# Kernel tuning notes

Hardware: AMD Instinct MI355X
Metric: run time of the kernel (lower is better)

The kernel has to match this reference:

```python
import jax, jax.numpy as jnp
import numpy as np

# Conv2d config matching init_kwargs
STRIDE = (1, 1)
PADDING = (1, 1)
DILATION = (1, 1)


def setup_inputs() -> dict:
    key = jax.random.key(0)
    k1, k2, k3 = jax.random.split(key, 3)
    B, Cin, H, W_ = 32, 128, 56, 56
    Cout, KH, KW = 256, 3, 3
    x = jax.random.normal(k1, (B, Cin, H, W_), dtype=jnp.float32)
    # original init: uniform(-stdv, stdv), stdv = 1/sqrt(Cin*KH*KW)
    stdv = 1.0 / np.sqrt(Cin * KH * KW)
    W = jax.random.uniform(k2, (Cout, Cin, KH, KW), dtype=jnp.float32, minval=-stdv, maxval=stdv)
    b = jax.random.uniform(k3, (Cout,), dtype=jnp.float32, minval=-stdv, maxval=stdv)
    return {"x": x, "W": W, "b": b}


def reference(x, W, b):
    # Same math as unfold(im2col) + GEMM + bias: a standard 2D convolution.
    out = jax.lax.conv_general_dilated(
        x, W,
        window_strides=STRIDE,
        padding=[(PADDING[0], PADDING[0]), (PADDING[1], PADDING[1])],
        rhs_dilation=DILATION,
        dimension_numbers=("NCHW", "OIHW", "NCHW"),
    )
    return out + b[None, :, None, None]
```

## Files before the change

kernel.cpp:

```cpp
#include <hip/hip_runtime.h>

typedef unsigned short ushort_t;
typedef __attribute__((ext_vector_type(8))) short bf16x8;
typedef __attribute__((ext_vector_type(4))) float f32x4;
typedef __attribute__((ext_vector_type(4))) unsigned short ushort4v;

constexpr int BATCH = 32, CIN = 128, H = 56, W = 56, COUT = 256;
constexpr int HP = 58, WP = 58;
constexpr int KTOT = CIN * 9;
constexpr size_t WB_BYTES = (size_t)COUT * KTOT * 2;
constexpr int PLANE = BATCH * HP * WP;
constexpr size_t XP_BYTES = (size_t)16 * PLANE * 8 * 2;

__device__ inline ushort_t f2bf(float f) {
  union { float fl; unsigned u; } v; v.fl = f;
  unsigned u = v.u;
  return (ushort_t)((u + 0x7fffu + ((u >> 16) & 1u)) >> 16);
}


__global__ void conv_w(const float* __restrict__ Ws, ushort_t* __restrict__ Wb2) {
  int idx = blockIdx.x * 256 + threadIdx.x;
  int c = idx & 7;
  int cout = (idx >> 3) & 255;
  int kb = (idx >> 11) & 7;
  int t = idx >> 14;
  int pos = t >> 1, half = t & 1;
  int cin = half * 64 + kb * 8 + c;
  Wb2[idx] = f2bf(Ws[(cout * 128 + cin) * 9 + pos]);
}

__global__ void xpad2(const float* __restrict__ x, ushort_t* __restrict__ xp2) {
  __shared__ ushort_t tile[128][58];
  int bh = blockIdx.x;
  int b = bh / 58, h = bh - b * 58;
  bool interior = (h >= 1 && h <= 56);
  if (interior) {
    int hIn = h - 1;
    const float4* x4 = (const float4*)x;
    {
      int ch = threadIdx.x & 127, side = threadIdx.x >> 7;
      tile[ch][side * 57] = 0;
    }
    for (int it = 0; it < 7; ++it) {
      int i = it * 256 + (int)threadIdx.x;
      int ch = i / 14, q = i - ch * 14;
      float4 v = x4[(size_t)(b * 128 + ch) * 784 + hIn * 14 + q];
      int wb = 1 + q * 4;
      tile[ch][wb + 0] = f2bf(v.x);
      tile[ch][wb + 1] = f2bf(v.y);
      tile[ch][wb + 2] = f2bf(v.z);
      tile[ch][wb + 3] = f2bf(v.w);
    }
  }
  __syncthreads();
  ushort4v* o4 = (ushort4v*)xp2;
  for (int it = 0; it < 8; ++it) {
    int i = it * 256 + (int)threadIdx.x;
    if (i >= 1856) break;
    int c8 = i / 116, r = i - c8 * 116;
    int w = r >> 1, hf = r & 1;
    ushort4v v;
    if (interior) {
      int ch = c8 * 8 + hf * 4;
      v.x = tile[ch + 0][w];
      v.y = tile[ch + 1][w];
      v.z = tile[ch + 2][w];
      v.w = tile[ch + 3][w];
    } else {
      v.x = v.y = v.z = v.w = 0;
    }
    o4[((size_t)((c8 * 32 + b) * 58 + h) * 58 + w) * 2 + hf] = v;
  }
}


__global__ __launch_bounds__(512) void conv_mfma(
    const ushort_t* __restrict__ Wb2, const ushort_t* __restrict__ xp2,
    const float* __restrict__ bias, float* __restrict__ out) {
  __shared__ ushort_t ldsA[2][16384];
  __shared__ ushort_t ldsB[2][16384];

  const int tid = threadIdx.x;
  const int lane = tid & 63;
  const int wid = tid >> 6;
  const int wm = wid >> 2, wn = wid & 3;
  const int lg = lane >> 4, lr = lane & 15;
  const int tileN = blockIdx.x;

  const ushort_t* aSrc[4];
  const ushort_t* bSrc[4];
#pragma unroll
  for (int p = 0; p < 4; ++p) {
    int idx = p * 512 + tid;
    aSrc[p] = Wb2 + idx * 8;
    int kb = idx >> 8, pi = idx & 255;
    int pg = tileN * 256 + pi;
    int bq = pg / 3136;
    int rem = pg - bq * 3136;
    int hh = rem / 56;
    int ww = rem - hh * 56;
    int pixBase = (bq * 58 + hh) * 58 + ww;
    bSrc[p] = xp2 + ((size_t)kb * PLANE + pixBase) * 8;
  }
  const int dOff = tid * 8;

  auto stage = [&](int bb, int t) {
    int pos = t >> 1;
    int kh = pos / 3;
    int kw = pos - kh * 3;
    int aoff = t * 16384;
    int boff = (t & 1) * (8 * PLANE * 8) + (kh * 58 + kw) * 8;
    ushort_t* dA = &ldsA[bb][0];
    ushort_t* dB = &ldsB[bb][0];
#pragma unroll
    for (int p = 0; p < 4; ++p) {
      __builtin_amdgcn_global_load_lds(
          (const __attribute__((address_space(1))) unsigned int*)(aSrc[p] + aoff),
          (__attribute__((address_space(3))) unsigned int*)(dA + p * 4096 + dOff),
          16, 0, 0);
      __builtin_amdgcn_global_load_lds(
          (const __attribute__((address_space(1))) unsigned int*)(bSrc[p] + boff),
          (__attribute__((address_space(3))) unsigned int*)(dB + p * 4096 + dOff),
          16, 0, 0);
    }
  };

  f32x4 acc[8][4] = {};

  stage(0, 0);
  stage(1, 1);
  asm volatile("s_waitcnt vmcnt(8)" ::: "memory");
  __builtin_amdgcn_s_barrier();

  for (int t = 0; t < 18; ++t) {
    const int p = t & 1;
    const ushort_t* A0 = &ldsA[p][0];
    const ushort_t* B0 = &ldsB[p][0];

    bf16x8 a0[8], b0[4];
    {
      const int kb = lg;
#pragma unroll
      for (int m = 0; m < 8; ++m)
        a0[m] = *(const bf16x8*)(A0 + kb * 2048 + (wm * 128 + m * 16 + lr) * 8);
#pragma unroll
      for (int n = 0; n < 4; ++n)
        b0[n] = *(const bf16x8*)(B0 + kb * 2048 + (wn * 64 + n * 16 + lr) * 8);
    }
#pragma unroll
    for (int m = 0; m < 8; ++m)
#pragma unroll
      for (int n = 0; n < 4; ++n)
        acc[m][n] = __builtin_amdgcn_mfma_f32_16x16x32_bf16(a0[m], b0[n], acc[m][n], 0, 0, 0);

    bf16x8 a1[8], b1[4];
    {
      const int kb = 4 + lg;
#pragma unroll
      for (int m = 0; m < 8; ++m)
        a1[m] = *(const bf16x8*)(A0 + kb * 2048 + (wm * 128 + m * 16 + lr) * 8);
#pragma unroll
      for (int n = 0; n < 4; ++n)
        b1[n] = *(const bf16x8*)(B0 + kb * 2048 + (wn * 64 + n * 16 + lr) * 8);
    }

    asm volatile("s_waitcnt lgkmcnt(0)" ::: "memory");
    __builtin_amdgcn_sched_barrier(0);
    __builtin_amdgcn_s_barrier();
    __builtin_amdgcn_sched_barrier(0);
    if (t < 16) stage(p, t + 2);

    __builtin_amdgcn_s_setprio(1);
#pragma unroll
    for (int m = 0; m < 8; ++m)
#pragma unroll
      for (int n = 0; n < 4; ++n)
        acc[m][n] = __builtin_amdgcn_mfma_f32_16x16x32_bf16(a1[m], b1[n], acc[m][n], 0, 0, 0);
    __builtin_amdgcn_s_setprio(0);

    if (t < 16) {
      asm volatile("s_waitcnt vmcnt(8)" ::: "memory");
    } else if (t == 16) {
      asm volatile("s_waitcnt vmcnt(0)" ::: "memory");
    }
    __builtin_amdgcn_s_barrier();
  }

  const int cb = wm * 128 + lg * 4;
  float bvv[8][4];
#pragma unroll
  for (int m = 0; m < 8; ++m)
#pragma unroll
    for (int r = 0; r < 4; ++r) bvv[m][r] = bias[cb + m * 16 + r];

#pragma unroll
  for (int n = 0; n < 4; ++n) {
    int pgo = tileN * 256 + wn * 64 + n * 16 + lr;
    int bq2 = pgo / 3136;
    int rem2 = pgo - bq2 * 3136;
    float* op = out + (size_t)bq2 * 256 * 3136 + rem2;
#pragma unroll
    for (int m = 0; m < 8; ++m)
#pragma unroll
      for (int r = 0; r < 4; ++r)
        op[(size_t)(cb + m * 16 + r) * 3136] = acc[m][n][r] + bvv[m][r];
  }
}

__global__ void conv_naive(const float* __restrict__ x, const float* __restrict__ Wt,
                           const float* __restrict__ bias, float* __restrict__ out, int total) {
  int idx = blockIdx.x * 256 + threadIdx.x;
  if (idx >= total) return;
  int w = idx % 56;
  int t1 = idx / 56;
  int h = t1 % 56;
  int t2 = t1 / 56;
  int co = t2 % 256;
  int b = t2 / 256;
  float acc = bias[co];
  for (int c = 0; c < 128; ++c)
    for (int kh = 0; kh < 3; ++kh) {
      int ih = h + kh - 1;
      if (ih < 0 || ih >= 56) continue;
      for (int kw = 0; kw < 3; ++kw) {
        int iw = w + kw - 1;
        if (iw < 0 || iw >= 56) continue;
        acc += x[((b * 128 + c) * 56 + ih) * 56 + iw] * Wt[((co * 128 + c) * 3 + kh) * 3 + kw];
      }
    }
  out[idx] = acc;
}

extern "C" void kernel_launch(void* const* d_in, const int* in_sizes, int n_in,
                              void* d_out, int out_size, void* d_ws, size_t ws_size,
                              hipStream_t stream) {
  const float* x = (const float*)d_in[0];
  const float* Wt = (const float*)d_in[1];
  const float* bias = (const float*)d_in[2];
  float* out = (float*)d_out;

  const size_t need = WB_BYTES + XP_BYTES;
  if (ws_size < need) {
    int total = BATCH * COUT * H * W;
    conv_naive<<<(total + 255) / 256, 256, 0, stream>>>(x, Wt, bias, out, total);
    return;
  }
  ushort_t* Wb2 = (ushort_t*)d_ws;
  ushort_t* xp2 = (ushort_t*)((char*)d_ws + WB_BYTES);

  conv_w<<<1152, 256, 0, stream>>>(Wt, Wb2);
  xpad2<<<32 * 58, 256, 0, stream>>>(x, xp2);
  conv_mfma<<<392, 512, 0, stream>>>(Wb2, xp2, bias, out);
}
```

Before: 213.3 us.

## Restructure conv GEMM mainloop into four-phase half-K pipeline with 4-slot LDS ring

Replaces the double-buffered full-K-tile staging with a ring of four half-K slots in one LDS array. Each iteration is split into four phases, each loading A/B fragments for half the M rows and issuing the global-to-LDS loads for a future half-stage, so copies interleave more finely with MFMA work. This adds more barriers per iteration and changes the vmcnt wait accounting, which could add sync overhead or stalls.

```diff
diff --git a/kernel.cpp b/kernel.cpp
--- a/kernel.cpp
+++ b/kernel.cpp
@@ -78,8 +78,7 @@
 __global__ __launch_bounds__(512) void conv_mfma(
     const ushort_t* __restrict__ Wb2, const ushort_t* __restrict__ xp2,
     const float* __restrict__ bias, float* __restrict__ out) {
-  __shared__ ushort_t ldsA[2][16384];
-  __shared__ ushort_t ldsB[2][16384];
+  __shared__ ushort_t lds[65536];
 
   const int tid = threadIdx.x;
   const int lane = tid & 63;
@@ -88,104 +87,105 @@
   const int lg = lane >> 4, lr = lane & 15;
   const int tileN = blockIdx.x;
 
-  const ushort_t* aSrc[4];
-  const ushort_t* bSrc[4];
-#pragma unroll
-  for (int p = 0; p < 4; ++p) {
-    int idx = p * 512 + tid;
-    aSrc[p] = Wb2 + idx * 8;
-    int kb = idx >> 8, pi = idx & 255;
-    int pg = tileN * 256 + pi;
+  const int rowOff = (tid & 255) * 8;
+  const int kb2lo = tid >> 8;
+  const ushort_t* bThr;
+  {
+    int pg = tileN * 256 + (tid & 255);
     int bq = pg / 3136;
     int rem = pg - bq * 3136;
     int hh = rem / 56;
     int ww = rem - hh * 56;
-    int pixBase = (bq * 58 + hh) * 58 + ww;
-    bSrc[p] = xp2 + ((size_t)kb * PLANE + pixBase) * 8;
-  }
-  const int dOff = tid * 8;
-
-  auto stage = [&](int bb, int t) {
-    int pos = t >> 1;
-    int kh = pos / 3;
-    int kw = pos - kh * 3;
-    int aoff = t * 16384;
-    int boff = (t & 1) * (8 * PLANE * 8) + (kh * 58 + kw) * 8;
-    ushort_t* dA = &ldsA[bb][0];
-    ushort_t* dB = &ldsB[bb][0];
-#pragma unroll
-    for (int p = 0; p < 4; ++p) {
-      __builtin_amdgcn_global_load_lds(
-          (const __attribute__((address_space(1))) unsigned int*)(aSrc[p] + aoff),
-          (__attribute__((address_space(3))) unsigned int*)(dA + p * 4096 + dOff),
-          16, 0, 0);
-      __builtin_amdgcn_global_load_lds(
-          (const __attribute__((address_space(1))) unsigned int*)(bSrc[p] + boff),
-          (__attribute__((address_space(3))) unsigned int*)(dB + p * 4096 + dOff),
-          16, 0, 0);
+    int pixChunk = (bq * 58 + hh) * 58 + ww;
+    bThr = xp2 + ((size_t)kb2lo * PLANE + pixChunk) * 8;
+  }
+
+  const int aBaseT = (lg * 256 + wm * 128 + lr) * 8;
+  const int bBaseT = (lg * 256 + wn * 64 + lr) * 8 + 8192;
+
+  auto stageUnit = [&](int hs, int part) {
+    int ts = hs >> 1, kss = hs & 1;
+    int rs = (hs & 3) * 16384;
+    if (part == 0) {
+      int base = (ts * 8 + kss * 4) * 2048;
+#pragma unroll
+      for (int pl = 0; pl < 2; ++pl) {
+        int kb2 = pl * 2 + kb2lo;
+        __builtin_amdgcn_global_load_lds(
+            (const __attribute__((address_space(1))) unsigned int*)(Wb2 + base + kb2 * 2048 + rowOff),
+            (__attribute__((address_space(3))) unsigned int*)(lds + rs + kb2 * 2048 + rowOff),
+            16, 0, 0);
+      }
+    } else {
+      int pos = ts >> 1;
+      int kh = pos / 3, kw = pos - kh * 3;
+      size_t off = ((size_t)((ts & 1) * 8 + kss * 4) * PLANE) * 8 + (kh * 58 + kw) * 8;
+#pragma unroll
+      for (int pl = 0; pl < 2; ++pl) {
+        int kb2 = pl * 2 + kb2lo;
+        __builtin_amdgcn_global_load_lds(
+            (const __attribute__((address_space(1))) unsigned int*)(bThr + off + (size_t)pl * 2 * PLANE * 8),
+            (__attribute__((address_space(3))) unsigned int*)(lds + rs + 8192 + kb2 * 2048 + rowOff),
+            16, 0, 0);
+      }
     }
   };
 
   f32x4 acc[8][4] = {};
-
-  stage(0, 0);
-  stage(1, 1);
-  asm volatile("s_waitcnt vmcnt(8)" ::: "memory");
+  bf16x8 bfr[4];
+
+#define DO_PHASE(KS, MH)                                                       \
+  {                                                                            \
+    const int rb = ((2 * t + (KS)) & 3) * 16384;                               \
+    if ((MH) == 0) {                                                           \
+      _Pragma("unroll")                                                        \
+      for (int n = 0; n < 4; ++n)                                              \
+        bfr[n] = *(const bf16x8*)(lds + rb + bBaseT + n * 128);                \
+    }                                                                          \
+    bf16x8 afr[4];                                                             \
+    _Pragma("unroll")                                                          \
+    for (int i = 0; i < 4; ++i)                                                \
+      afr[i] = *(const bf16x8*)(lds + rb + aBaseT + ((MH)*4 + i) * 128);       \
+    {                                                                          \
+      int hs = 2 * t + (KS) + 2;                                               \
+      if (hs < 36) stageUnit(hs, (MH));                                        \
+    }                                                                          \
+    __builtin_amdgcn_s_barrier();                                              \
+    asm volatile("s_waitcnt lgkmcnt(0)" ::: "memory");                         \
+    __builtin_amdgcn_s_setprio(1);                                             \
+    _Pragma("unroll")                                                          \
+    for (int i = 0; i < 4; ++i)                                                \
+      _Pragma("unroll")                                                        \
+      for (int n = 0; n < 4; ++n)                                              \
+        acc[(MH)*4 + i][n] =                                                   \
+            __builtin_amdgcn_mfma_f32_16x16x32_bf16(afr[i], bfr[n],            \
+                                                    acc[(MH)*4 + i][n], 0, 0, 0); \
+    __builtin_amdgcn_s_setprio(0);                                             \
+  }
+
+  stageUnit(0, 0);
+  stageUnit(0, 1);
+  stageUnit(1, 0);
+  stageUnit(1, 1);
+  asm volatile("s_waitcnt vmcnt(0)" ::: "memory");
   __builtin_amdgcn_s_barrier();
 
   for (int t = 0; t < 18; ++t) {
-    const int p = t & 1;
-    const ushort_t* A0 = &ldsA[p][0];
-    const ushort_t* B0 = &ldsB[p][0];
-
-    bf16x8 a0[8], b0[4];
-    {
-      const int kb = lg;
-#pragma unroll
-      for (int m = 0; m < 8; ++m)
-        a0[m] = *(const bf16x8*)(A0 + kb * 2048 + (wm * 128 + m * 16 + lr) * 8);
-#pragma unroll
-      for (int n = 0; n < 4; ++n)
-        b0[n] = *(const bf16x8*)(B0 + kb * 2048 + (wn * 64 + n * 16 + lr) * 8);
-    }
-#pragma unroll
-    for (int m = 0; m < 8; ++m)
-#pragma unroll
-      for (int n = 0; n < 4; ++n)
-        acc[m][n] = __builtin_amdgcn_mfma_f32_16x16x32_bf16(a0[m], b0[n], acc[m][n], 0, 0, 0);
-
-    bf16x8 a1[8], b1[4];
-    {
-      const int kb = 4 + lg;
-#pragma unroll
-      for (int m = 0; m < 8; ++m)
-        a1[m] = *(const bf16x8*)(A0 + kb * 2048 + (wm * 128 + m * 16 + lr) * 8);
-#pragma unroll
-      for (int n = 0; n < 4; ++n)
-        b1[n] = *(const bf16x8*)(B0 + kb * 2048 + (wn * 64 + n * 16 + lr) * 8);
-    }
-
-    asm volatile("s_waitcnt lgkmcnt(0)" ::: "memory");
-    __builtin_amdgcn_sched_barrier(0);
-    __builtin_amdgcn_s_barrier();
-    __builtin_amdgcn_sched_barrier(0);
-    if (t < 16) stage(p, t + 2);
-
-    __builtin_amdgcn_s_setprio(1);
-#pragma unroll
-    for (int m = 0; m < 8; ++m)
-#pragma unroll
-      for (int n = 0; n < 4; ++n)
-        acc[m][n] = __builtin_amdgcn_mfma_f32_16x16x32_bf16(a1[m], b1[n], acc[m][n], 0, 0, 0);
-    __builtin_amdgcn_s_setprio(0);
-
+    DO_PHASE(0, 0)
+    __builtin_amdgcn_s_barrier();
+    DO_PHASE(0, 1)
+    __builtin_amdgcn_s_barrier();
+    DO_PHASE(1, 0)
+    __builtin_amdgcn_s_barrier();
+    DO_PHASE(1, 1)
     if (t < 16) {
-      asm volatile("s_waitcnt vmcnt(8)" ::: "memory");
+      asm volatile("s_waitcnt vmcnt(4)" ::: "memory");
     } else if (t == 16) {
       asm volatile("s_waitcnt vmcnt(0)" ::: "memory");
     }
     __builtin_amdgcn_s_barrier();
   }
+#undef DO_PHASE
 
   const int cb = wm * 128 + lg * 4;
   float bvv[8][4];
```

New measurement: 215.0 us. About the same (+0.8%).

## Switch conv GEMM to 32x32x16 MFMA tiles and remap block order

Applied to the files above, without the earlier changes.

Replaces the 16x16x32 bf16 MFMA inner loop with 32x32x16 MFMAs, so each wave holds 4x2 larger accumulator tiles instead of 8x4 small ones. This reduces LDS fragment reads and the MFMA instruction count per K-step. It also permutes blockIdx into tileN, interleaving blocks across eight groups, likely to spread work across XCDs and improve cache locality. The epilogue is rewritten for the 32x32 output register layout and reads bias per element instead of preloading it.

```diff
diff --git a/kernel.cpp b/kernel.cpp
--- a/kernel.cpp
+++ b/kernel.cpp
@@ -2,7 +2,7 @@
 
 typedef unsigned short ushort_t;
 typedef __attribute__((ext_vector_type(8))) short bf16x8;
-typedef __attribute__((ext_vector_type(4))) float f32x4;
+typedef __attribute__((ext_vector_type(16))) float f32x16;
 typedef __attribute__((ext_vector_type(4))) unsigned short ushort4v;
 
 constexpr int BATCH = 32, CIN = 128, H = 56, W = 56, COUT = 256;
@@ -85,8 +85,8 @@
   const int lane = tid & 63;
   const int wid = tid >> 6;
   const int wm = wid >> 2, wn = wid & 3;
-  const int lg = lane >> 4, lr = lane & 15;
-  const int tileN = blockIdx.x;
+  const int l5 = lane >> 5, l31 = lane & 31;
+  const int tileN = ((int)blockIdx.x & 7) * 49 + ((int)blockIdx.x >> 3);
 
   const ushort_t* aSrc[4];
   const ushort_t* bSrc[4];
@@ -126,7 +126,10 @@
     }
   };
 
-  f32x4 acc[8][4] = {};
+  f32x16 acc[4][2] = {};
+
+  const int aBase = (wm * 128 + l31) * 8;
+  const int bBase = (wn * 64 + l31) * 8;
 
   stage(0, 0);
   stage(1, 1);
@@ -138,31 +141,36 @@
     const ushort_t* A0 = &ldsA[p][0];
     const ushort_t* B0 = &ldsB[p][0];
 
-    bf16x8 a0[8], b0[4];
-    {
-      const int kb = lg;
-#pragma unroll
-      for (int m = 0; m < 8; ++m)
-        a0[m] = *(const bf16x8*)(A0 + kb * 2048 + (wm * 128 + m * 16 + lr) * 8);
-#pragma unroll
-      for (int n = 0; n < 4; ++n)
-        b0[n] = *(const bf16x8*)(B0 + kb * 2048 + (wn * 64 + n * 16 + lr) * 8);
-    }
-#pragma unroll
-    for (int m = 0; m < 8; ++m)
-#pragma unroll
-      for (int n = 0; n < 4; ++n)
-        acc[m][n] = __builtin_amdgcn_mfma_f32_16x16x32_bf16(a0[m], b0[n], acc[m][n], 0, 0, 0);
-
-    bf16x8 a1[8], b1[4];
-    {
-      const int kb = 4 + lg;
-#pragma unroll
-      for (int m = 0; m < 8; ++m)
-        a1[m] = *(const bf16x8*)(A0 + kb * 2048 + (wm * 128 + m * 16 + lr) * 8);
-#pragma unroll
-      for (int n = 0; n < 4; ++n)
-        b1[n] = *(const bf16x8*)(B0 + kb * 2048 + (wn * 64 + n * 16 + lr) * 8);
+    bf16x8 a01[2][4], b01[2][2];
+#pragma unroll
+    for (int ks = 0; ks < 2; ++ks) {
+      const int kb = (ks * 2 + l5) * 2048;
+#pragma unroll
+      for (int mu = 0; mu < 4; ++mu)
+        a01[ks][mu] = *(const bf16x8*)(A0 + kb + aBase + mu * 256);
+#pragma unroll
+      for (int nu = 0; nu < 2; ++nu)
+        b01[ks][nu] = *(const bf16x8*)(B0 + kb + bBase + nu * 256);
+    }
+#pragma unroll
+    for (int ks = 0; ks < 2; ++ks)
+#pragma unroll
+      for (int mu = 0; mu < 4; ++mu)
+#pragma unroll
+        for (int nu = 0; nu < 2; ++nu)
+          acc[mu][nu] = __builtin_amdgcn_mfma_f32_32x32x16_bf16(
+              a01[ks][mu], b01[ks][nu], acc[mu][nu], 0, 0, 0);
+
+    bf16x8 a23[2][4], b23[2][2];
+#pragma unroll
+    for (int ks = 0; ks < 2; ++ks) {
+      const int kb = ((ks + 2) * 2 + l5) * 2048;
+#pragma unroll
+      for (int mu = 0; mu < 4; ++mu)
+        a23[ks][mu] = *(const bf16x8*)(A0 + kb + aBase + mu * 256);
+#pragma unroll
+      for (int nu = 0; nu < 2; ++nu)
+        b23[ks][nu] = *(const bf16x8*)(B0 + kb + bBase + nu * 256);
     }
 
     asm volatile("s_waitcnt lgkmcnt(0)" ::: "memory");
@@ -173,10 +181,13 @@
 
     __builtin_amdgcn_s_setprio(1);
 #pragma unroll
-    for (int m = 0; m < 8; ++m)
-#pragma unroll
-      for (int n = 0; n < 4; ++n)
-        acc[m][n] = __builtin_amdgcn_mfma_f32_16x16x32_bf16(a1[m], b1[n], acc[m][n], 0, 0, 0);
+    for (int ks = 0; ks < 2; ++ks)
+#pragma unroll
+      for (int mu = 0; mu < 4; ++mu)
+#pragma unroll
+        for (int nu = 0; nu < 2; ++nu)
+          acc[mu][nu] = __builtin_amdgcn_mfma_f32_32x32x16_bf16(
+              a23[ks][mu], b23[ks][nu], acc[mu][nu], 0, 0, 0);
     __builtin_amdgcn_s_setprio(0);
 
     if (t < 16) {
@@ -187,24 +198,19 @@
     __builtin_amdgcn_s_barrier();
   }
 
-  const int cb = wm * 128 + lg * 4;
-  float bvv[8][4];
-#pragma unroll
-  for (int m = 0; m < 8; ++m)
-#pragma unroll
-    for (int r = 0; r < 4; ++r) bvv[m][r] = bias[cb + m * 16 + r];
-
-#pragma unroll
-  for (int n = 0; n < 4; ++n) {
-    int pgo = tileN * 256 + wn * 64 + n * 16 + lr;
+#pragma unroll
+  for (int nu = 0; nu < 2; ++nu) {
+    int pgo = tileN * 256 + wn * 64 + nu * 32 + l31;
     int bq2 = pgo / 3136;
     int rem2 = pgo - bq2 * 3136;
     float* op = out + (size_t)bq2 * 256 * 3136 + rem2;
 #pragma unroll
-    for (int m = 0; m < 8; ++m)
-#pragma unroll
-      for (int r = 0; r < 4; ++r)
-        op[(size_t)(cb + m * 16 + r) * 3136] = acc[m][n][r] + bvv[m][r];
+    for (int mu = 0; mu < 4; ++mu)
+#pragma unroll
+      for (int r = 0; r < 16; ++r) {
+        int co = wm * 128 + mu * 32 + (r & 3) + 8 * (r >> 2) + 4 * l5;
+        op[(size_t)co * 3136] = acc[mu][nu][r] + bias[co];
+      }
   }
 }
 
```

Result: slower. 218.4 us (+2.4%).

## Software-pipeline LDS fragment loads across iterations and request two blocks per CU

Applied to the files above, without the earlier changes.

Restructures the main loop so the first-half fragments for the next stage are loaded from LDS after the barrier and overlap with the second-half MFMAs. Each MFMA batch now runs on fragments that were already loaded, hiding LDS latency. It also sets launch_bounds to (512,2) and computes load addresses from one base pointer instead of per-iteration arrays, which lowers register use. The occupancy hint caps registers and could cause spills with 32 accumulators plus 24 fragment registers. With LDS at 128KB per block, two blocks may not fit on a CU anyway.

```diff
diff --git a/kernel.cpp b/kernel.cpp
--- a/kernel.cpp
+++ b/kernel.cpp
@@ -75,7 +75,7 @@
 }
 
 
-__global__ __launch_bounds__(512) void conv_mfma(
+__global__ __launch_bounds__(512, 2) void conv_mfma(
     const ushort_t* __restrict__ Wb2, const ushort_t* __restrict__ xp2,
     const float* __restrict__ bias, float* __restrict__ out) {
   __shared__ ushort_t ldsA[2][16384];
@@ -88,20 +88,16 @@
   const int lg = lane >> 4, lr = lane & 15;
   const int tileN = blockIdx.x;
 
-  const ushort_t* aSrc[4];
-  const ushort_t* bSrc[4];
-#pragma unroll
-  for (int p = 0; p < 4; ++p) {
-    int idx = p * 512 + tid;
-    aSrc[p] = Wb2 + idx * 8;
-    int kb = idx >> 8, pi = idx & 255;
-    int pg = tileN * 256 + pi;
+  const ushort_t* aSrc0 = Wb2 + tid * 8;
+  const ushort_t* bSrc0;
+  {
+    int pg = tileN * 256 + (tid & 255);
     int bq = pg / 3136;
     int rem = pg - bq * 3136;
     int hh = rem / 56;
     int ww = rem - hh * 56;
     int pixBase = (bq * 58 + hh) * 58 + ww;
-    bSrc[p] = xp2 + ((size_t)kb * PLANE + pixBase) * 8;
+    bSrc0 = xp2 + ((size_t)(tid >> 8) * PLANE + pixBase) * 8;
   }
   const int dOff = tid * 8;
 
@@ -109,60 +105,62 @@
     int pos = t >> 1;
     int kh = pos / 3;
     int kw = pos - kh * 3;
-    int aoff = t * 16384;
-    int boff = (t & 1) * (8 * PLANE * 8) + (kh * 58 + kw) * 8;
+    const ushort_t* aS = aSrc0 + t * 16384;
+    const ushort_t* bS = bSrc0 + (t & 1) * (size_t)(8 * PLANE * 8) + (kh * 58 + kw) * 8;
     ushort_t* dA = &ldsA[bb][0];
     ushort_t* dB = &ldsB[bb][0];
 #pragma unroll
     for (int p = 0; p < 4; ++p) {
       __builtin_amdgcn_global_load_lds(
-          (const __attribute__((address_space(1))) unsigned int*)(aSrc[p] + aoff),
+          (const __attribute__((address_space(1))) unsigned int*)(aS + p * 4096),
           (__attribute__((address_space(3))) unsigned int*)(dA + p * 4096 + dOff),
           16, 0, 0);
       __builtin_amdgcn_global_load_lds(
-          (const __attribute__((address_space(1))) unsigned int*)(bSrc[p] + boff),
+          (const __attribute__((address_space(1))) unsigned int*)(bS + (size_t)p * (2 * PLANE * 8)),
           (__attribute__((address_space(3))) unsigned int*)(dB + p * 4096 + dOff),
           16, 0, 0);
     }
   };
 
   f32x4 acc[8][4] = {};
+  bf16x8 af0[8], bf0[4], af1[8], bf1[4];
+
+  const int aOffT = (wm * 128 + lr) * 8;
+  const int bOffT = (wn * 64 + lr) * 8;
 
   stage(0, 0);
   stage(1, 1);
   asm volatile("s_waitcnt vmcnt(8)" ::: "memory");
   __builtin_amdgcn_s_barrier();
+  {
+    const ushort_t* A0 = &ldsA[0][0];
+    const ushort_t* B0 = &ldsB[0][0];
+    const int kb = lg * 2048;
+#pragma unroll
+    for (int m = 0; m < 8; ++m) af0[m] = *(const bf16x8*)(A0 + kb + aOffT + m * 128);
+#pragma unroll
+    for (int n = 0; n < 4; ++n) bf0[n] = *(const bf16x8*)(B0 + kb + bOffT + n * 128);
+  }
 
   for (int t = 0; t < 18; ++t) {
     const int p = t & 1;
     const ushort_t* A0 = &ldsA[p][0];
     const ushort_t* B0 = &ldsB[p][0];
 
-    bf16x8 a0[8], b0[4];
+    __builtin_amdgcn_s_setprio(1);
+#pragma unroll
+    for (int m = 0; m < 8; ++m)
+#pragma unroll
+      for (int n = 0; n < 4; ++n)
+        acc[m][n] = __builtin_amdgcn_mfma_f32_16x16x32_bf16(af0[m], bf0[n], acc[m][n], 0, 0, 0);
+    __builtin_amdgcn_s_setprio(0);
+
     {
-      const int kb = lg;
-#pragma unroll
-      for (int m = 0; m < 8; ++m)
-        a0[m] = *(const bf16x8*)(A0 + kb * 2048 + (wm * 128 + m * 16 + lr) * 8);
-#pragma unroll
-      for (int n = 0; n < 4; ++n)
-        b0[n] = *(const bf16x8*)(B0 + kb * 2048 + (wn * 64 + n * 16 + lr) * 8);
-    }
-#pragma unroll
-    for (int m = 0; m < 8; ++m)
-#pragma unroll
-      for (int n = 0; n < 4; ++n)
-        acc[m][n] = __builtin_amdgcn_mfma_f32_16x16x32_bf16(a0[m], b0[n], acc[m][n], 0, 0, 0);
-
-    bf16x8 a1[8], b1[4];
-    {
-      const int kb = 4 + lg;
-#pragma unroll
-      for (int m = 0; m < 8; ++m)
-        a1[m] = *(const bf16x8*)(A0 + kb * 2048 + (wm * 128 + m * 16 + lr) * 8);
-#pragma unroll
-      for (int n = 0; n < 4; ++n)
-        b1[n] = *(const bf16x8*)(B0 + kb * 2048 + (wn * 64 + n * 16 + lr) * 8);
+      const int kb = (4 + lg) * 2048;
+#pragma unroll
+      for (int m = 0; m < 8; ++m) af1[m] = *(const bf16x8*)(A0 + kb + aOffT + m * 128);
+#pragma unroll
+      for (int n = 0; n < 4; ++n) bf1[n] = *(const bf16x8*)(B0 + kb + bOffT + n * 128);
     }
 
     asm volatile("s_waitcnt lgkmcnt(0)" ::: "memory");
@@ -171,20 +169,30 @@
     __builtin_amdgcn_sched_barrier(0);
     if (t < 16) stage(p, t + 2);
 
-    __builtin_amdgcn_s_setprio(1);
-#pragma unroll
-    for (int m = 0; m < 8; ++m)
-#pragma unroll
-      for (int n = 0; n < 4; ++n)
-        acc[m][n] = __builtin_amdgcn_mfma_f32_16x16x32_bf16(a1[m], b1[n], acc[m][n], 0, 0, 0);
-    __builtin_amdgcn_s_setprio(0);
-
     if (t < 16) {
       asm volatile("s_waitcnt vmcnt(8)" ::: "memory");
-    } else if (t == 16) {
+    } else {
       asm volatile("s_waitcnt vmcnt(0)" ::: "memory");
     }
     __builtin_amdgcn_s_barrier();
+
+    __builtin_amdgcn_s_setprio(1);
+#pragma unroll
+    for (int m = 0; m < 8; ++m)
+#pragma unroll
+      for (int n = 0; n < 4; ++n)
+        acc[m][n] = __builtin_amdgcn_mfma_f32_16x16x32_bf16(af1[m], bf1[n], acc[m][n], 0, 0, 0);
+    __builtin_amdgcn_s_setprio(0);
+
+    if (t < 17) {
+      const ushort_t* A1 = &ldsA[p ^ 1][0];
+      const ushort_t* B1 = &ldsB[p ^ 1][0];
+      const int kb = lg * 2048;
+#pragma unroll
+      for (int m = 0; m < 8; ++m) af0[m] = *(const bf16x8*)(A1 + kb + aOffT + m * 128);
+#pragma unroll
+      for (int n = 0; n < 4; ++n) bf0[n] = *(const bf16x8*)(B1 + kb + bOffT + n * 128);
+    }
   }
 
   const int cb = wm * 128 + lg * 4;
```

After: 218.2 us. 2.3% more time.
